# Performance work log

Hardware: AMD Instinct MI355X
Metric: run time of the kernel (lower is better)

The kernel has to match this reference:

```python
import jax, jax.numpy as jnp
import numpy as np

H = 48; W = 48; C_IN = 32; C_OUT = 64
L = 4                      # liftsamples
RADIUS = 3                 # neighborhood radius
CMCO = 16                  # LieConv PointConv fixed mid channels
FOCAL = W / np.pi          # equidistant fisheye focal
CX, CY = (W - 1) / 2.0, (H - 1) / 2.0
EPS = 1e-7


def _build_neighbor_indices(h, w, radius):
    offs = [(dx, dy) for dy in range(-radius, radius + 1)
            for dx in range(-radius, radius + 1)
            if dx * dx + dy * dy <= radius * radius]
    offs = np.array(offs, dtype=np.int64)  # (k,2) as (dx,dy)
    yy, xx = np.meshgrid(np.arange(h), np.arange(w), indexing='ij')
    yy = yy.reshape(-1, 1); xx = xx.reshape(-1, 1)
    ny = yy + offs[None, :, 1]; nx = xx + offs[None, :, 0]
    valid = (ny >= 0) & (ny < h) & (nx >= 0) & (nx < w)
    idx = ny * w + nx
    return np.where(valid, idx, -1).astype(np.int32)  # (h*w, k)


def swish(x):
    return x * jax.nn.sigmoid(x)


def so3_exp(wvec):
    # Rodrigues: (...,3) -> (...,3,3)
    th = jnp.maximum(jnp.linalg.norm(wvec, axis=-1, keepdims=True), EPS)
    k = wvec / th
    kx, ky, kz = k[..., 0], k[..., 1], k[..., 2]
    z = jnp.zeros_like(kx)
    K = jnp.stack([jnp.stack([z, -kz, ky], -1),
                   jnp.stack([kz, z, -kx], -1),
                   jnp.stack([-ky, kx, z], -1)], -2)
    th = th[..., None]
    I = jnp.eye(3, dtype=wvec.dtype)
    return I + jnp.sin(th) * K + (1.0 - jnp.cos(th)) * (K @ K)


def so3_log(R):
    # (...,3,3) -> (...,3)
    tr = R[..., 0, 0] + R[..., 1, 1] + R[..., 2, 2]
    cos = jnp.clip((tr - 1.0) * 0.5, -1.0 + 1e-6, 1.0 - 1e-6)
    th = jnp.arccos(cos)
    v = jnp.stack([R[..., 2, 1] - R[..., 1, 2],
                   R[..., 0, 2] - R[..., 2, 0],
                   R[..., 1, 0] - R[..., 0, 1]], -1)
    return v * (th / (2.0 * jnp.sin(th)))[..., None]


def setup_inputs() -> dict:
    key = jax.random.key(0)
    ks = jax.random.split(key, 6)
    def lin(k, fi, fo):
        return jax.random.normal(k, (fi, fo), jnp.float32) / np.sqrt(fi)
    return {
        'x': jax.random.normal(ks[0], (2, C_IN, H, W), jnp.float32),
        'neighbor_idx': jnp.asarray(_build_neighbor_indices(H, W, RADIUS)),
        'W1': lin(ks[1], 3, 32), 'b1': jnp.zeros((32,), jnp.float32),
        'W2': lin(ks[2], 32, 32), 'b2': jnp.zeros((32,), jnp.float32),
        'W3': lin(ks[3], 32, CMCO), 'b3': jnp.zeros((CMCO,), jnp.float32),
        'Wl': lin(ks[4], CMCO * C_IN, C_OUT), 'bl': jnp.zeros((C_OUT,), jnp.float32),
    }


def _lift_log(dtype):
    # pixel grid -> unit rays -> so(3) log of lifted group elems, shape (n*L, 3)
    u = jnp.arange(W, dtype=dtype); v = jnp.arange(H, dtype=dtype)
    uu, vv = jnp.meshgrid(u, v)               # 'xy' indexing, (H,W)
    dx = (uu - CX).reshape(-1); dy = (vv - CY).reshape(-1)
    r = jnp.sqrt(dx * dx + dy * dy)
    theta = r / FOCAL
    rs = jnp.maximum(r, EPS)
    rays = jnp.stack([jnp.sin(theta) * dx / rs,
                      jnp.sin(theta) * dy / rs,
                      jnp.cos(theta)], -1)    # (n,3)
    pz = jnp.clip(rays[:, 2], -1.0 + 1e-6, 1.0 - 1e-6)
    ang = jnp.arccos(pz)
    axis = jnp.stack([-rays[:, 1], rays[:, 0], jnp.zeros_like(pz)], -1)
    axis = axis / jnp.maximum(jnp.linalg.norm(axis, axis=-1, keepdims=True), EPS)
    Rp = so3_exp(axis * ang[:, None])          # (n,3,3), Rp @ e3 = ray
    alphas = jnp.arange(L, dtype=dtype) * (2.0 * np.pi / L)
    Rz = so3_exp(jnp.stack([jnp.zeros_like(alphas), jnp.zeros_like(alphas), alphas], -1))
    Rlift = jnp.einsum('nij,ljk->nlik', Rp, Rz)  # (n,L,3,3)
    return so3_log(Rlift).reshape(H * W * L, 3)


def reference(x, neighbor_idx, W1, b1, W2, b2, W3, b3, Wl, bl):
    bs, c, h, w = x.shape
    n = h * w
    k = neighbor_idx.shape[1]
    nL, K = n * L, k * L

    a = _lift_log(x.dtype)                                   # (nL,3)

    valid = neighbor_idx >= 0                                # (n,k)
    safe_pix = jnp.maximum(neighbor_idx, 0).astype(jnp.int32)
    # lifted neighbor indices: query lift copy l sees all (j, l') neighbors
    nb_lift = safe_pix[:, None, :, None] * L + jnp.arange(L, dtype=jnp.int32)[None, None, None, :]
    nb_lift = jnp.broadcast_to(nb_lift, (n, L, k, L)).reshape(nL, K)
    nb_pix = jnp.broadcast_to(safe_pix[:, None, :, None], (n, L, k, L)).reshape(nL, K)
    mask = jnp.broadcast_to(valid[:, None, :, None], (n, L, k, L)).reshape(nL, K)

    # pairwise group elements: log(exp(-b) @ exp(a))
    b_log = a[nb_lift]                                       # (nL,K,3)
    Rab = jnp.einsum('qmij,qjk->qmik', so3_exp(-b_log), so3_exp(a))
    ab = so3_log(Rab)                                        # (nL,K,3)

    # kernel MLP (WeightNet: 3 -> 32 -> 32 -> 16, swish)
    hdn = swish(ab @ W1 + b1)
    hdn = swish(hdn @ W2 + b2)
    wts = swish(hdn @ W3 + b3)                               # (nL,K,16)
    wts = jnp.where(mask[..., None], wts, 0.0)

    values = x.transpose(0, 2, 3, 1).reshape(bs, n, c)       # (bs,n,c)
    nv = values[:, nb_pix]                                   # (bs,nL,K,c)
    partial = jnp.einsum('bqmc,qmf->bqcf', nv, wts).reshape(bs, nL, c * CMCO)
    out = partial @ Wl + bl                                  # (bs,nL,c_out)
    out = out.reshape(bs, n, L, -1).mean(axis=2)             # pool over lift samples
    return out.reshape(bs, h, w, -1).transpose(0, 3, 1, 2)   # (bs,c_out,h,w)
```

## Files before the change

kernel.cpp:

```cpp
#include <hip/hip_runtime.h>

#define WW   48
#define NPIX 2304
#define CIN  32
#define COUT 64
#define KNB  29
#define FCO  16
#define NPJ  (NPIX * KNB)
#define GEN_WAVES  ((NPJ + 6) / 7)
#define GEN_BLOCKS ((GEN_WAVES + 3) / 4)
#define NEDGE (NPIX * 6 + 1)

#define WS_RP64 0
#define WS_EAB  165888
#define WS_EG   248832
#define WS_M0   1133568
#define WS_V    1133632
#define WS_PART 4340800

__device__ __forceinline__ float swish_f(float x) {
    return x * __builtin_amdgcn_rcpf(1.0f + __expf(-x));
}

__device__ __forceinline__ void so3_exp_d(double wx, double wy, double wz, double R[9]) {
    double n  = sqrt(wx * wx + wy * wy + wz * wz);
    double th = fmax(n, 1e-7);
    double kx = wx / th, ky = wy / th, kz = wz / th;
    double s = sin(th), c = cos(th);
    double omc = 1.0 - c;
    R[0] = 1.0 + omc * (kx * kx - 1.0);
    R[1] = -s * kz + omc * kx * ky;
    R[2] =  s * ky + omc * kx * kz;
    R[3] =  s * kz + omc * kx * ky;
    R[4] = 1.0 + omc * (ky * ky - 1.0);
    R[5] = -s * kx + omc * ky * kz;
    R[6] = -s * ky + omc * kz * kx;
    R[7] =  s * kx + omc * kz * ky;
    R[8] = 1.0 + omc * (kz * kz - 1.0);
}

__device__ __forceinline__ void compute_Rp_d(int p, double R[9]) {
    int ui = p % WW, vi = p / WW;
    double dx = (double)ui - 23.5;
    double dy = (double)vi - 23.5;
    double r  = sqrt(dx * dx + dy * dy);
    const double FOCAL = 48.0 / 3.14159265358979323846;
    double theta = r / FOCAL;
    double rs = fmax(r, 1e-7);
    double st = sin(theta);
    double rayx = st * dx / rs;
    double rayy = st * dy / rs;
    double rayz = cos(theta);
    double pz  = fmin(fmax(rayz, -1.0 + 1e-6), 1.0 - 1e-6);
    double ang = acos(pz);
    double ax = -rayy, ay = rayx;
    double an = fmax(sqrt(ax * ax + ay * ay), 1e-7);
    ax /= an; ay /= an;
    so3_exp_d(ax * ang, ay * ang, 0.0, R);
}

__device__ __forceinline__ void mlp_half(float ab0, float ab1, float ab2, const int Q0,
    const float* __restrict__ W1, const float* __restrict__ b1,
    const float* __restrict__ W2, const float* __restrict__ b2,
    const float* __restrict__ W3, const float* __restrict__ b3,
    float* acc3) {
    float accq[16];
    #pragma unroll
    for (int q = 0; q < 16; ++q) accq[q] = b2[Q0 + q];
    #pragma unroll
    for (int i = 0; i < 32; ++i) {
        float h = swish_f(b1[i] + ab0 * W1[i] + ab1 * W1[32 + i] + ab2 * W1[64 + i]);
        #pragma unroll
        for (int q = 0; q < 16; ++q) accq[q] += h * W2[i * 32 + Q0 + q];
    }
    #pragma unroll
    for (int q = 0; q < 16; ++q) {
        float h2 = swish_f(accq[q]);
        #pragma unroll
        for (int f = 0; f < FCO; ++f) acc3[f] += h2 * W3[(Q0 + q) * FCO + f];
    }
}

__device__ __forceinline__ void mlp_eval(float ab0, float ab1, float ab2,
    const float* __restrict__ W1, const float* __restrict__ b1,
    const float* __restrict__ W2, const float* __restrict__ b2,
    const float* __restrict__ W3, const float* __restrict__ b3,
    float* o) {
    float acc3[FCO];
    #pragma unroll
    for (int f = 0; f < FCO; ++f) acc3[f] = b3[f];
    mlp_half(ab0, ab1, ab2, 0,  W1, b1, W2, b2, W3, b3, acc3);
    __builtin_amdgcn_sched_barrier(0);
    mlp_half(ab0, ab1, ab2, 16, W1, b1, W2, b2, W3, b3, acc3);
    #pragma unroll
    for (int f = 0; f < FCO; ++f) o[f] = swish_f(acc3[f]);
}

__global__ __launch_bounds__(256)
void rp_kernel(double* __restrict__ rp64, float* __restrict__ eab) {
    int tid = blockIdx.x * 256 + threadIdx.x;
    if (tid >= NPIX * 4) return;
    int p = tid >> 2, which = tid & 3;
    double R[9];
    compute_Rp_d(p, R);
    if (which == 0) {
        #pragma unroll
        for (int e = 0; e < 9; ++e) rp64[p * 9 + e] = R[e];
    } else {
        int m = which - 1;
        int l = m + (m >> 1);
        double c = (l == 0) ? 1.0 : 0.0;
        double s = (l == 1) ? 1.0 : ((l == 3) ? -1.0 : 0.0);
        double M[9];
        #pragma unroll
        for (int i = 0; i < 3; ++i) {
            M[i * 3 + 0] =  R[i * 3 + 0] * c + R[i * 3 + 1] * s;
            M[i * 3 + 1] = -R[i * 3 + 0] * s + R[i * 3 + 1] * c;
            M[i * 3 + 2] =  R[i * 3 + 2];
        }
        double tr   = M[0] + M[4] + M[8];
        double cosv = fmin(fmax((tr - 1.0) * 0.5, -1.0 + 1e-6), 1.0 - 1e-6);
        double th   = acos(cosv);
        double sv   = sqrt((1.0 - cosv) * (1.0 + cosv));
        double fac  = th / (2.0 * sv);
        eab[p * 9 + m * 3 + 0] = (float)((M[7] - M[5]) * fac);
        eab[p * 9 + m * 3 + 1] = (float)((M[2] - M[6]) * fac);
        eab[p * 9 + m * 3 + 2] = (float)((M[3] - M[1]) * fac);
    }
}

__global__ __launch_bounds__(256)
void vlog2_kernel(const int* __restrict__ nbr, const double* __restrict__ rp64,
                  float* __restrict__ vws) {
    int tid = blockIdx.x * 256 + threadIdx.x;
    if (tid >= NPJ * 4) return;
    int g2 = tid >> 2;
    int d  = tid & 3;
    int p = g2 / KNB, j = g2 - p * KNB;
    int pj = max(nbr[p * KNB + j], 0);
    double Rq[9];
    #pragma unroll
    for (int q = 0; q < 9; ++q) Rq[q] = rp64[p * 9 + q];
    double X[9];
    #pragma unroll
    for (int q = 0; q < 9; ++q) X[q] = 0.0;
    #pragma unroll
    for (int k = 0; k < 3; ++k) {
        double rn0 = rp64[pj * 9 + k * 3 + 0];
        double rn1 = rp64[pj * 9 + k * 3 + 1];
        double rn2 = rp64[pj * 9 + k * 3 + 2];
        #pragma unroll
        for (int jj = 0; jj < 3; ++jj) {
            X[0 * 3 + jj] += rn0 * Rq[k * 3 + jj];
            X[1 * 3 + jj] += rn1 * Rq[k * 3 + jj];
            X[2 * 3 + jj] += rn2 * Rq[k * 3 + jj];
        }
    }
    double c = (d == 0) ? 1.0 : ((d == 2) ? -1.0 : 0.0);
    double s = (d == 1) ? 1.0 : ((d == 3) ? -1.0 : 0.0);
    double M0 =  X[0] * c + X[1] * s;
    double M1 = -X[0] * s + X[1] * c;
    double M2 =  X[2];
    double M3 =  X[3] * c + X[4] * s;
    double M4 = -X[3] * s + X[4] * c;
    double M5 =  X[5];
    double M6 =  X[6] * c + X[7] * s;
    double M7 = -X[6] * s + X[7] * c;
    double M8 =  X[8];
    double tr   = M0 + M4 + M8;
    double cosv = fmin(fmax((tr - 1.0) * 0.5, -1.0 + 1e-6), 1.0 - 1e-6);
    double th   = acos(cosv);
    double svv  = sqrt((1.0 - cosv) * (1.0 + cosv));
    double fac  = th / (2.0 * svv);
    float* dst = vws + g2 * 12 + d * 3;
    dst[0] = (float)((M7 - M5) * fac);
    dst[1] = (float)((M2 - M6) * fac);
    dst[2] = (float)((M3 - M1) * fac);
}

__global__ __launch_bounds__(256)
void edge_kernel(const float* __restrict__ W1, const float* __restrict__ b1,
                 const float* __restrict__ W2, const float* __restrict__ b2,
                 const float* __restrict__ W3, const float* __restrict__ b3,
                 const float* __restrict__ eab,
                 float* __restrict__ eg, float* __restrict__ m0v) {
    int tid = blockIdx.x * 256 + threadIdx.x;
    int g  = tid >> 2;
    int ql = tid & 3;
    if (g >= NEDGE) return;
    bool isz = (g == NPIX * 6);
    int gc = isz ? 0 : g;
    int pix = gc / 6, which = gc - pix * 6;
    int m = (which < 3) ? which : (which - 3);
    float sg = isz ? 0.f : ((which < 3) ? 1.f : -1.f);
    const float* ep = eab + pix * 9 + m * 3;
    float ab0 = sg * ep[0], ab1 = sg * ep[1], ab2 = sg * ep[2];
    const int Q0 = ql * 8;
    float accq[8];
    #pragma unroll
    for (int q = 0; q < 8; ++q) accq[q] = b2[Q0 + q];
    #pragma unroll
    for (int i = 0; i < 32; ++i) {
        float h = swish_f(b1[i] + ab0 * W1[i] + ab1 * W1[32 + i] + ab2 * W1[64 + i]);
        #pragma unroll
        for (int q = 0; q < 8; ++q) accq[q] += h * W2[i * 32 + Q0 + q];
    }
    float part3[FCO];
    #pragma unroll
    for (int f = 0; f < FCO; ++f) part3[f] = 0.f;
    #pragma unroll
    for (int q = 0; q < 8; ++q) {
        float h2 = swish_f(accq[q]);
        #pragma unroll
        for (int f = 0; f < FCO; ++f) part3[f] += h2 * W3[(Q0 + q) * FCO + f];
    }
    #pragma unroll
    for (int f = 0; f < FCO; ++f) {
        float a = part3[f];
        a += __shfl_xor(a, 1);
        a += __shfl_xor(a, 2);
        part3[f] = a;
    }
    if (ql == 0) {
        float* dst = isz ? m0v : (eg + g * FCO);
        #pragma unroll
        for (int f = 0; f < FCO; ++f) dst[f] = swish_f(b3[f] + part3[f]);
    }
}

__global__ __launch_bounds__(256)
void mlp1_kernel(const float* __restrict__ W1, const float* __restrict__ b1,
                 const float* __restrict__ W2, const float* __restrict__ b2,
                 const float* __restrict__ W3, const float* __restrict__ b3,
                 const float* __restrict__ vws, float* __restrict__ part) {
    int wave = blockIdx.x * 4 + (threadIdx.x >> 6);
    int lane = threadIdx.x & 63;
    int slot = lane / 9;
    int e    = lane - slot * 9;
    int g2   = wave * 7 + slot;
    int g2c  = min(g2, NPJ - 1);
    int l1m = e / 3, l2m = e - l1m * 3;
    int l1 = l1m + (l1m >> 1);
    int l2 = l2m + (l2m >> 1);
    int d  = (l1 - l2) & 3;
    const float* vp = vws + g2c * 12 + d * 3;
    float v0 = vp[0], v1 = vp[1], v2 = vp[2];
    float ab0 = (l2m == 0) ? v0 : ((l2m == 1) ?  v1 : -v1);
    float ab1 = (l2m == 0) ? v1 : ((l2m == 1) ? -v0 :  v0);
    float o[FCO];
    mlp_eval(ab0, ab1, v2, W1, b1, W2, b2, W3, b3, o);
    #pragma unroll
    for (int f = 0; f < FCO; ++f) {
        float a = o[f];
        a += __shfl(a, min(lane + 1, 63)) + __shfl(a, min(lane + 2, 63));
        a += __shfl(a, min(lane + 3, 63)) + __shfl(a, min(lane + 6, 63));
        o[f] = a;
    }
    if (e == 0 && lane < 63 && g2 < NPJ) {
        float* dst = part + g2 * FCO;
        #pragma unroll
        for (int f = 0; f < FCO; ++f) dst[f] = o[f];
    }
}

__global__ __launch_bounds__(256)
void agg_kernel(const float* __restrict__ x, const int* __restrict__ nbr,
                const float* __restrict__ Wl, const float* __restrict__ bl,
                const float* __restrict__ eg, const float* __restrict__ m0v,
                const float* __restrict__ part, float* __restrict__ out) {
    __shared__ int   spj[KNB];
    __shared__ int   sval[KNB];
    __shared__ float sE[FCO];
    __shared__ float sS[KNB][FCO];
    __shared__ float sxv[2][CIN][KNB];
    __shared__ float sT[2][CIN][FCO];
    __shared__ float spp[256];

    const int p = blockIdx.x;
    const int t = threadIdx.x;

    if (t < KNB) {
        int idx = nbr[p * KNB + t];
        spj[t]  = max(idx, 0);
        sval[t] = (idx >= 0) ? 1 : 0;
    } else if (t >= 32 && t < 32 + FCO) {
        int f = t - 32;
        sE[f] = eg[(p * 6 + 0) * FCO + f] + eg[(p * 6 + 1) * FCO + f]
              + eg[(p * 6 + 2) * FCO + f] + m0v[f];
    }
    __syncthreads();

    for (int e = t; e < 2 * CIN * KNB; e += 256) {
        int bb = e / (CIN * KNB);
        int r  = e - bb * (CIN * KNB);
        int c  = r / KNB;
        int j  = r - c * KNB;
        sxv[bb][c][j] = x[bb * (CIN * NPIX) + c * NPIX + spj[j]];
    }
    for (int idx = t; idx < KNB * FCO; idx += 256) {
        int j = idx >> 4, f = idx & 15;
        float acc = part[(p * KNB + j) * FCO + f];
        int n6 = spj[j] * 6;
        acc += eg[(n6 + 3) * FCO + f] + eg[(n6 + 4) * FCO + f] + eg[(n6 + 5) * FCO + f];
        acc += sE[f];
        sS[j][f] = sval[j] ? acc * 0.25f : 0.f;
    }
    __syncthreads();

    for (int tt = t; tt < 2 * CIN * FCO; tt += 256) {
        int bb = tt >> 9;
        int c  = (tt >> 4) & 31;
        int f  = tt & 15;
        float acc = 0.f;
        #pragma unroll
        for (int j = 0; j < KNB; ++j)
            acc += sxv[bb][c][j] * sS[j][f];
        sT[bb][c][f] = acc;
    }
    __syncthreads();

    if (t < 128) {
        int half = t >> 6, co = t & 63;
        const float* Tb0 = &sT[0][0][0];
        const float* Tb1 = &sT[1][0][0];
        float a0 = 0.f, a1 = 0.f;
        int cf0 = half * 256;
        #pragma unroll 8
        for (int cf = cf0; cf < cf0 + 256; ++cf) {
            float w = Wl[cf * COUT + co];
            a0 += Tb0[cf] * w;
            a1 += Tb1[cf] * w;
        }
        spp[half * 128 + 0 * 64 + co] = a0;
        spp[half * 128 + 1 * 64 + co] = a1;
    }
    __syncthreads();
    if (t < 128) {
        int bb = t >> 6, co = t & 63;
        out[bb * (COUT * NPIX) + co * NPIX + p] =
            spp[0 * 128 + bb * 64 + co] + spp[1 * 128 + bb * 64 + co] + bl[co];
    }
}

extern "C" void kernel_launch(void* const* d_in, const int* in_sizes, int n_in,
                              void* d_out, int out_size, void* d_ws, size_t ws_size,
                              hipStream_t stream) {
    const float* x  = (const float*)d_in[0];
    const int* nbr  = (const int*)d_in[1];
    const float* W1 = (const float*)d_in[2];
    const float* b1 = (const float*)d_in[3];
    const float* W2 = (const float*)d_in[4];
    const float* b2 = (const float*)d_in[5];
    const float* W3 = (const float*)d_in[6];
    const float* b3 = (const float*)d_in[7];
    const float* Wl = (const float*)d_in[8];
    const float* bl = (const float*)d_in[9];
    float* out = (float*)d_out;

    char* ws = (char*)d_ws;
    double* rp64 = (double*)(ws + WS_RP64);
    float*  eab  = (float*)(ws + WS_EAB);
    float*  eg   = (float*)(ws + WS_EG);
    float*  m0v  = (float*)(ws + WS_M0);
    float*  vws  = (float*)(ws + WS_V);
    float*  part = (float*)(ws + WS_PART);

    hipLaunchKernelGGL(rp_kernel, dim3((NPIX * 4 + 255) / 256), dim3(256), 0, stream,
                       rp64, eab);
    hipLaunchKernelGGL(vlog2_kernel, dim3((NPJ * 4 + 255) / 256), dim3(256), 0, stream,
                       nbr, rp64, vws);
    hipLaunchKernelGGL(edge_kernel, dim3((NEDGE * 4 + 255) / 256), dim3(256), 0, stream,
                       W1, b1, W2, b2, W3, b3, eab, eg, m0v);
    hipLaunchKernelGGL(mlp1_kernel, dim3(GEN_BLOCKS), dim3(256), 0, stream,
                       W1, b1, W2, b2, W3, b3, vws, part);
    hipLaunchKernelGGL(agg_kernel, dim3(NPIX), dim3(256), 0, stream,
                       x, nbr, Wl, bl, eg, m0v, part, out);
}
```

Before: 86.29 us.

## Process four pixels per aggregation block and stage Wl tiles in shared memory

The aggregation kernel now handles four output pixels per block instead of one, so each 64x64 chunk of the final linear weight Wl is loaded once into shared memory and reused across four pixels and both batches. The final projection is restructured so each thread accumulates a 2x4 register tile over a 16-row split, followed by a shared-memory reduction. This targets redundant global reads of the 128 KB Wl matrix, which the old layout repeated for every pixel, and the poor utilisation of the 128-thread matvec. In exchange the grid shrinks to 576 blocks, shared memory use grows, and more barriers are added per block.

```diff
diff --git a/kernel.cpp b/kernel.cpp
--- a/kernel.cpp
+++ b/kernel.cpp
@@ -10,6 +10,8 @@
 #define GEN_WAVES  ((NPJ + 6) / 7)
 #define GEN_BLOCKS ((GEN_WAVES + 3) / 4)
 #define NEDGE (NPIX * 6 + 1)
+#define PIXT 4
+#define AGG_BLOCKS (NPIX / PIXT)
 
 #define WS_RP64 0
 #define WS_EAB  165888
@@ -268,77 +270,112 @@
                 const float* __restrict__ Wl, const float* __restrict__ bl,
                 const float* __restrict__ eg, const float* __restrict__ m0v,
                 const float* __restrict__ part, float* __restrict__ out) {
-    __shared__ int   spj[KNB];
-    __shared__ int   sval[KNB];
-    __shared__ float sE[FCO];
-    __shared__ float sS[KNB][FCO];
-    __shared__ float sxv[2][CIN][KNB];
-    __shared__ float sT[2][CIN][FCO];
-    __shared__ float spp[256];
-
-    const int p = blockIdx.x;
-    const int t = threadIdx.x;
-
-    if (t < KNB) {
-        int idx = nbr[p * KNB + t];
-        spj[t]  = max(idx, 0);
-        sval[t] = (idx >= 0) ? 1 : 0;
-    } else if (t >= 32 && t < 32 + FCO) {
-        int f = t - 32;
-        sE[f] = eg[(p * 6 + 0) * FCO + f] + eg[(p * 6 + 1) * FCO + f]
-              + eg[(p * 6 + 2) * FCO + f] + m0v[f];
+    __shared__ int   spj[PIXT][KNB];
+    __shared__ int   sval[PIXT][KNB];
+    __shared__ float sE[PIXT][FCO];
+    __shared__ float sS[PIXT][KNB][FCO];
+    __shared__ float sxv[PIXT][CIN][KNB + 1];
+    __shared__ float sT[512][2 * PIXT + 2];
+    __shared__ float swl[64][64];
+
+    const int p0 = blockIdx.x * PIXT;
+    const int t  = threadIdx.x;
+
+    if (t < PIXT * KNB) {
+        int pix = t / KNB, j = t - pix * KNB;
+        int idx = nbr[(p0 + pix) * KNB + j];
+        spj[pix][j]  = max(idx, 0);
+        sval[pix][j] = (idx >= 0) ? 1 : 0;
+    } else if (t >= 128 && t < 128 + PIXT * FCO) {
+        int pf = t - 128;
+        int pix = pf >> 4, f = pf & 15;
+        int p6 = (p0 + pix) * 6;
+        sE[pix][f] = eg[(p6 + 0) * FCO + f] + eg[(p6 + 1) * FCO + f]
+                   + eg[(p6 + 2) * FCO + f] + m0v[f];
     }
     __syncthreads();
 
-    for (int e = t; e < 2 * CIN * KNB; e += 256) {
-        int bb = e / (CIN * KNB);
-        int r  = e - bb * (CIN * KNB);
-        int c  = r / KNB;
-        int j  = r - c * KNB;
-        sxv[bb][c][j] = x[bb * (CIN * NPIX) + c * NPIX + spj[j]];
-    }
-    for (int idx = t; idx < KNB * FCO; idx += 256) {
-        int j = idx >> 4, f = idx & 15;
-        float acc = part[(p * KNB + j) * FCO + f];
-        int n6 = spj[j] * 6;
+    for (int idx = t; idx < PIXT * KNB * FCO; idx += 256) {
+        int f = idx & 15;
+        int jj = idx >> 4;
+        int pix = jj / KNB, j = jj - pix * KNB;
+        float acc = part[((p0 + pix) * KNB + j) * FCO + f];
+        int n6 = spj[pix][j] * 6;
         acc += eg[(n6 + 3) * FCO + f] + eg[(n6 + 4) * FCO + f] + eg[(n6 + 5) * FCO + f];
-        acc += sE[f];
-        sS[j][f] = sval[j] ? acc * 0.25f : 0.f;
+        acc += sE[pix][f];
+        sS[pix][j][f] = sval[pix][j] ? acc * 0.25f : 0.f;
     }
     __syncthreads();
 
-    for (int tt = t; tt < 2 * CIN * FCO; tt += 256) {
-        int bb = tt >> 9;
-        int c  = (tt >> 4) & 31;
-        int f  = tt & 15;
-        float acc = 0.f;
-        #pragma unroll
-        for (int j = 0; j < KNB; ++j)
-            acc += sxv[bb][c][j] * sS[j][f];
-        sT[bb][c][f] = acc;
-    }
+    for (int b = 0; b < 2; ++b) {
+        for (int idx = t; idx < PIXT * CIN * KNB; idx += 256) {
+            int j = idx % KNB;
+            int cc = idx / KNB;
+            int c = cc & 31, pix = cc >> 5;
+            sxv[pix][c][j] = x[b * (CIN * NPIX) + c * NPIX + spj[pix][j]];
+        }
+        __syncthreads();
+        for (int idx = t; idx < PIXT * CIN * FCO; idx += 256) {
+            int f = idx & 15;
+            int c = (idx >> 4) & 31;
+            int pix = idx >> 9;
+            float acc = 0.f;
+            #pragma unroll
+            for (int j = 0; j < KNB; ++j)
+                acc += sxv[pix][c][j] * sS[pix][j][f];
+            sT[c * 16 + f][pix * 2 + b] = acc;
+        }
+        __syncthreads();
+    }
+
+    const int coq = t & 15;
+    const int pix = (t >> 4) & 3;
+    const int ss  = t >> 6;
+    float acc[2][4];
+    #pragma unroll
+    for (int b = 0; b < 2; ++b)
+        #pragma unroll
+        for (int q = 0; q < 4; ++q) acc[b][q] = 0.f;
+    for (int cc = 0; cc < 8; ++cc) {
+        for (int idx = t; idx < 64 * 64; idx += 256) {
+            int cfo = idx >> 6, co = idx & 63;
+            swl[cfo][co] = Wl[(cc * 64 + cfo) * COUT + co];
+        }
+        __syncthreads();
+        #pragma unroll
+        for (int k = 0; k < 16; ++k) {
+            int cfo = ss * 16 + k;
+            int cf  = cc * 64 + cfo;
+            float t0 = sT[cf][pix * 2 + 0];
+            float t1 = sT[cf][pix * 2 + 1];
+            const float* wq = &swl[cfo][coq * 4];
+            #pragma unroll
+            for (int q = 0; q < 4; ++q) {
+                float w = wq[q];
+                acc[0][q] += t0 * w;
+                acc[1][q] += t1 * w;
+            }
+        }
+        __syncthreads();
+    }
+
+    float* spp = &sxv[0][0][0];
+    #pragma unroll
+    for (int b = 0; b < 2; ++b)
+        #pragma unroll
+        for (int q = 0; q < 4; ++q)
+            spp[ss * 512 + pix * 128 + b * 64 + coq * 4 + q] = acc[b][q];
     __syncthreads();
-
-    if (t < 128) {
-        int half = t >> 6, co = t & 63;
-        const float* Tb0 = &sT[0][0][0];
-        const float* Tb1 = &sT[1][0][0];
-        float a0 = 0.f, a1 = 0.f;
-        int cf0 = half * 256;
-        #pragma unroll 8
-        for (int cf = cf0; cf < cf0 + 256; ++cf) {
-            float w = Wl[cf * COUT + co];
-            a0 += Tb0[cf] * w;
-            a1 += Tb1[cf] * w;
-        }
-        spp[half * 128 + 0 * 64 + co] = a0;
-        spp[half * 128 + 1 * 64 + co] = a1;
-    }
-    __syncthreads();
-    if (t < 128) {
-        int bb = t >> 6, co = t & 63;
-        out[bb * (COUT * NPIX) + co * NPIX + p] =
-            spp[0 * 128 + bb * 64 + co] + spp[1 * 128 + bb * 64 + co] + bl[co];
+    for (int oidx = t; oidx < PIXT * 2 * COUT; oidx += 256) {
+        int px = oidx >> 7;
+        int b  = (oidx >> 6) & 1;
+        int co = oidx & 63;
+        float a = spp[0 * 512 + px * 128 + b * 64 + co]
+                + spp[1 * 512 + px * 128 + b * 64 + co]
+                + spp[2 * 512 + px * 128 + b * 64 + co]
+                + spp[3 * 512 + px * 128 + b * 64 + co]
+                + bl[co];
+        out[b * (COUT * NPIX) + co * NPIX + (p0 + px)] = a;
     }
 }
 
@@ -373,6 +410,6 @@
                        W1, b1, W2, b2, W3, b3, eab, eg, m0v);
     hipLaunchKernelGGL(mlp1_kernel, dim3(GEN_BLOCKS), dim3(256), 0, stream,
                        W1, b1, W2, b2, W3, b3, vws, part);
-    hipLaunchKernelGGL(agg_kernel, dim3(NPIX), dim3(256), 0, stream,
+    hipLaunchKernelGGL(agg_kernel, dim3(AGG_BLOCKS), dim3(256), 0, stream,
                        x, nbr, Wl, bl, eg, m0v, part, out);
 }
```

New measurement: 125.7 us. +45.7%, slower.
